# Kernel tuning notes

Measured on AMD Instinct MI355X. Metric: run time of the kernel, lower is better.

Reference implementation:

```python
import jax, jax.numpy as jnp
import numpy as np

N_NODES = 50000
N_EDGES = 400000
N_GRAPHS = 64
DN = 64    # node features
DE = 64    # edge features
DG = 16    # global features
DH = 128   # mlp hidden
DO = 64    # mlp output
NHID = 2   # hidden layers
E_IN = 2 * DN + DE + DG   # 208
N_IN = DN + DO + DG       # 144


def _mlp_params(key, d_in, d_h, d_out, n_hid):
    ks = jax.random.split(key, 3)
    w_in = jax.random.normal(ks[0], (d_in, d_h), jnp.float32) * (2.0 / d_in) ** 0.5
    w_h = jax.random.normal(ks[1], (n_hid, d_h, d_h), jnp.float32) * (2.0 / d_h) ** 0.5
    w_out = jax.random.normal(ks[2], (d_h, d_out), jnp.float32) * (2.0 / d_h) ** 0.5
    return (w_in, jnp.zeros((d_h,), jnp.float32), w_h, jnp.zeros((n_hid, d_h), jnp.float32),
            w_out, jnp.zeros((d_out,), jnp.float32), jnp.ones((d_out,), jnp.float32),
            jnp.zeros((d_out,), jnp.float32))


def _mlp(h, w_in, b_in, w_h, b_h, w_out, b_out, g, b):
    # Lin -> [relu, Lin]*NHID -> relu -> Lin -> LayerNorm  (dropout=0 at eval)
    h = h @ w_in + b_in
    for i in range(w_h.shape[0]):
        h = jax.nn.relu(h) @ w_h[i] + b_h[i]
    h = jax.nn.relu(h) @ w_out + b_out
    mu = jnp.mean(h, axis=-1, keepdims=True)
    var = jnp.mean((h - mu) ** 2, axis=-1, keepdims=True)
    return (h - mu) * jax.lax.rsqrt(var + 1e-5) * g + b


def setup_inputs() -> dict:
    key = jax.random.key(0)
    k = jax.random.split(key, 8)
    x = jax.random.normal(k[0], (N_NODES, DN), jnp.float32)
    edge_attr = jax.random.normal(k[1], (N_EDGES, DE), jnp.float32)
    u = jax.random.normal(k[2], (N_GRAPHS, DG), jnp.float32)
    edge_index = jax.random.randint(k[3], (2, N_EDGES), 0, N_NODES, dtype=jnp.int32)
    batch = jnp.sort(jax.random.randint(k[4], (N_NODES,), 0, N_GRAPHS, dtype=jnp.int32))
    names = ["w_in", "b_in", "w_h", "b_h", "w_out", "b_out", "ln_g", "ln_b"]
    d = {"x": x, "edge_attr": edge_attr, "u": u, "edge_index": edge_index, "batch": batch}
    for pref, kk, d_in in (("e_", k[5], E_IN), ("a_", k[6], E_IN), ("n_", k[7], N_IN)):
        for nm, v in zip(names, _mlp_params(kk, d_in, DH, DO, NHID)):
            d[pref + nm] = v
    return d


def reference(x, edge_attr, u, edge_index, batch,
              e_w_in, e_b_in, e_w_h, e_b_h, e_w_out, e_b_out, e_ln_g, e_ln_b,
              a_w_in, a_b_in, a_w_h, a_b_h, a_w_out, a_b_out, a_ln_g, a_ln_b,
              n_w_in, n_b_in, n_w_h, n_b_h, n_w_out, n_b_out, n_ln_g, n_ln_b):
    src, tgt = edge_index[0], edge_index[1]
    edge_batch = batch[src]
    # EdgeModel: gather src/tgt node feats + global feats, concat, MLP (+ sigmoid attention MLP)
    neigh = jnp.concatenate([x[src], x[tgt], edge_attr, u[edge_batch]], axis=1)  # [E, E_IN]
    e_out = _mlp(neigh, e_w_in, e_b_in, e_w_h, e_b_h, e_w_out, e_b_out, e_ln_g, e_ln_b)
    attn = jax.nn.sigmoid(_mlp(neigh, a_w_in, a_b_in, a_w_h, a_b_h, a_w_out, a_b_out, a_ln_g, a_ln_b))
    e_out = e_out * attn  # [E, DO]
    # NodeModel: scatter-sum incoming (target-indexed) edge outputs, concat, MLP
    agg = jax.ops.segment_sum(e_out, tgt, num_segments=x.shape[0])  # [N, DO], zeros for isolated nodes
    node_in = jnp.concatenate([x, agg, u[batch]], axis=1)  # [N, N_IN]
    x_out = _mlp(node_in, n_w_in, n_b_in, n_w_h, n_b_h, n_w_out, n_b_out, n_ln_g, n_ln_b)
    return x_out
```

## Files before the change

kernel.cpp:

```cpp
#include <hip/hip_runtime.h>
#include <math.h>

#define N_NODES 50000
#define N_EDGES 400000

typedef _Float16 half8 __attribute__((ext_vector_type(8)));
typedef float f32x4 __attribute__((ext_vector_type(4)));

#define LD1 232
#define LDH 136
#define LDN 168

#define AGG_OFF 0
#define XH_OFF  12800000
#define UH_OFF  19200000
#define WP_OFF  19202048
#define O_EW1 0
#define O_EH0 28672
#define O_EH1 45056
#define O_EWO 61440
#define O_AW1 69632
#define O_AH0 98304
#define O_AH1 114688
#define O_AWO 131072
#define O_NW1 139264
#define O_NH0 159744
#define O_NH1 176128
#define O_NWO 192512

__device__ __forceinline__ f32x4 mfma16(half8 a, half8 b, f32x4 c) {
  return __builtin_amdgcn_mfma_f32_16x16x32_f16(a, b, c, 0, 0, 0);
}

template<int NS, int LDSRC>
__device__ __forceinline__ void gemm32(const _Float16* __restrict__ src,
                                       _Float16* __restrict__ dst,
                                       const _Float16* __restrict__ wp16,
                                       const float* __restrict__ bias,
                                       int w, int lane) {
  const half8* wp = (const half8*)wp16;
  const int r = lane & 15, ch = lane >> 4;
  half8 B0[NS], B1[NS];
#pragma unroll
  for (int s = 0; s < NS; ++s) {
    B0[s] = wp[(s * 4 + ch) * 128 + w * 32 + r];
    B1[s] = wp[(s * 4 + ch) * 128 + w * 32 + 16 + r];
  }
  f32x4 a0[4], a1[4];
#pragma unroll
  for (int m = 0; m < 4; ++m) {
    a0[m] = (f32x4){0.f, 0.f, 0.f, 0.f};
    a1[m] = (f32x4){0.f, 0.f, 0.f, 0.f};
  }
#pragma unroll
  for (int s = 0; s < NS; ++s) {
#pragma unroll
    for (int m = 0; m < 4; ++m) {
      half8 a = *(const half8*)(src + (m * 16 + r) * LDSRC + s * 32 + ch * 8);
      a0[m] = mfma16(a, B0[s], a0[m]);
      a1[m] = mfma16(a, B1[s], a1[m]);
    }
  }
  float bb0 = bias[w * 32 + r], bb1 = bias[w * 32 + 16 + r];
#pragma unroll
  for (int m = 0; m < 4; ++m)
#pragma unroll
    for (int q = 0; q < 4; ++q) {
      int row = m * 16 + ch * 4 + q;
      dst[row * LDH + w * 32 + r]      = (_Float16)fmaxf(a0[m][q] + bb0, 0.f);
      dst[row * LDH + w * 32 + 16 + r] = (_Float16)fmaxf(a1[m][q] + bb1, 0.f);
    }
}

struct EdgeP {
  const float* edge_attr; const int* edge_index; const int* batch;
  const _Float16* x_h; const _Float16* u_h; const _Float16* wp;
  const float *eBin, *eBh, *eBout, *eG, *eBt;
  const float *aBin, *aBh, *aBout, *aG, *aBt;
  float* agg;
};

__global__ __launch_bounds__(512, 4) void edge_kernel(EdgeP p) {
  __shared__ __align__(16) _Float16 sIn[64 * LD1];
  __shared__ __align__(16) _Float16 sQe[64 * LDH];
  __shared__ __align__(16) _Float16 sQa[64 * LDH];
  __shared__ __align__(16) _Float16 sPa[64 * LDH];
  const int tid = threadIdx.x;
  const int e0 = blockIdx.x * 64;

  for (int idx = tid; idx < 64 * 32; idx += 512) {
    int c = idx & 31, e = idx >> 5;
    if (c >= 28) continue;
    int col = c * 8;
    half8 v;
    if (col < 64) {
      int s = p.edge_index[e0 + e];
      v = *(const half8*)(p.x_h + (size_t)s * 64 + col);
    } else if (col < 128) {
      int t = p.edge_index[N_EDGES + e0 + e];
      v = *(const half8*)(p.x_h + (size_t)t * 64 + col - 64);
    } else if (col < 192) {
      const float* ea = p.edge_attr + (size_t)(e0 + e) * 64 + (col - 128);
      float4 f0 = *(const float4*)ea, f1 = *(const float4*)(ea + 4);
      v[0] = (_Float16)f0.x; v[1] = (_Float16)f0.y;
      v[2] = (_Float16)f0.z; v[3] = (_Float16)f0.w;
      v[4] = (_Float16)f1.x; v[5] = (_Float16)f1.y;
      v[6] = (_Float16)f1.z; v[7] = (_Float16)f1.w;
    } else if (col < 208) {
      int s = p.edge_index[e0 + e];
      int eb = p.batch[s];
      v = *(const half8*)(p.u_h + eb * 16 + col - 192);
    } else {
#pragma unroll
      for (int j = 0; j < 8; ++j) v[j] = (_Float16)0.f;
    }
    *(half8*)(sIn + e * LD1 + col) = v;
  }
  __syncthreads();

  const int lane = tid & 63, wid = tid >> 6, we = wid & 3;
  const bool isE = wid < 4;
  _Float16* ping = isE ? sQe : sQa;
  _Float16* pong = isE ? sIn : sPa;
  const _Float16* w1 = p.wp + (isE ? O_EW1 : O_AW1);
  const _Float16* h0 = p.wp + (isE ? O_EH0 : O_AH0);
  const _Float16* h1 = p.wp + (isE ? O_EH1 : O_AH1);
  const _Float16* wo = p.wp + (isE ? O_EWO : O_AWO);
  const float* bin = isE ? p.eBin : p.aBin;
  const float* bh  = isE ? p.eBh  : p.aBh;
  const float* bo  = isE ? p.eBout: p.aBout;
  const float* g   = isE ? p.eG   : p.aG;
  const float* bt  = isE ? p.eBt  : p.aBt;

  gemm32<7, LD1>(sIn,  ping, w1, bin,      we, lane); __syncthreads();
  gemm32<4, LDH>(ping, pong, h0, bh,       we, lane); __syncthreads();
  gemm32<4, LDH>(pong, ping, h1, bh + 128, we, lane); __syncthreads();

  const int r = lane & 15, ch = lane >> 4;
  const half8* wpo = (const half8*)wo;
  half8 BO[4][4];
#pragma unroll
  for (int s = 0; s < 4; ++s)
#pragma unroll
    for (int t = 0; t < 4; ++t)
      BO[s][t] = wpo[(s * 4 + ch) * 64 + t * 16 + r];
  f32x4 acc[4];
#pragma unroll
  for (int t = 0; t < 4; ++t) acc[t] = (f32x4){0.f, 0.f, 0.f, 0.f};
#pragma unroll
  for (int s = 0; s < 4; ++s) {
    half8 a = *(const half8*)(ping + (we * 16 + r) * LDH + s * 32 + ch * 8);
#pragma unroll
    for (int t = 0; t < 4; ++t)
      acc[t] = mfma16(a, BO[s][t], acc[t]);
  }
  float gg[4], tt[4];
#pragma unroll
  for (int t = 0; t < 4; ++t) {
    int cidx = t * 16 + r;
    float bov = bo[cidx];
#pragma unroll
    for (int q = 0; q < 4; ++q) acc[t][q] += bov;
    gg[t] = g[cidx]; tt[t] = bt[cidx];
  }
  float mu_[4], rs_[4];
#pragma unroll
  for (int q = 0; q < 4; ++q) {
    float s1 = 0.f, s2 = 0.f;
#pragma unroll
    for (int t = 0; t < 4; ++t) { float v = acc[t][q]; s1 += v; s2 += v * v; }
#pragma unroll
    for (int mk = 1; mk < 16; mk <<= 1) {
      s1 += __shfl_xor(s1, mk); s2 += __shfl_xor(s2, mk);
    }
    mu_[q] = s1 * (1.f / 64);
    rs_[q] = rsqrtf(s2 * (1.f / 64) - mu_[q] * mu_[q] + 1e-5f);
  }
  float* cmb = (float*)sPa;
  if (!isE) {
#pragma unroll
    for (int q = 0; q < 4; ++q) {
      int row = we * 16 + ch * 4 + q;
#pragma unroll
      for (int t = 0; t < 4; ++t) {
        float oa = (acc[t][q] - mu_[q]) * rs_[q] * gg[t] + tt[t];
        cmb[row * 64 + t * 16 + r] = 1.f / (1.f + __expf(-oa));
      }
    }
  }
  __syncthreads();
  if (isE) {
#pragma unroll
    for (int q = 0; q < 4; ++q) {
      int row = we * 16 + ch * 4 + q;
      int tgt = p.edge_index[N_EDGES + e0 + row];
      float* ap = p.agg + (size_t)tgt * 64 + r;
#pragma unroll
      for (int t = 0; t < 4; ++t) {
        float oe = (acc[t][q] - mu_[q]) * rs_[q] * gg[t] + tt[t];
        atomicAdd(ap + t * 16, oe * cmb[row * 64 + t * 16 + r]);
      }
    }
  }
}

struct NodeP {
  const float* agg; const _Float16* x_h; const _Float16* u_h;
  const _Float16* wp; const int* batch;
  const float *Bin, *Bh, *Bout, *G, *Bt;
  float* out;
};

__global__ __launch_bounds__(256, 4) void node_kernel(NodeP p) {
  __shared__ __align__(16) _Float16 sIn[64 * LDN];
  __shared__ __align__(16) _Float16 sQ[64 * LDH];
  __shared__ int sB[64];
  const int tid = threadIdx.x;
  const int n0 = blockIdx.x * 64;

  if (tid < 64) {
    int n = n0 + tid;
    sB[tid] = (n < N_NODES) ? p.batch[n] : 0;
  }
  __syncthreads();

  for (int idx = tid; idx < 64 * 32; idx += 256) {
    int c = idx & 31, e = idx >> 5;
    if (c >= 21) continue;
    int n = n0 + e, col = c * 8;
    half8 v;
    if (n >= N_NODES || col >= 144) {
#pragma unroll
      for (int j = 0; j < 8; ++j) v[j] = (_Float16)0.f;
    } else if (col < 64) {
      v = *(const half8*)(p.x_h + (size_t)n * 64 + col);
    } else if (col < 128) {
      const float* ag = p.agg + (size_t)n * 64 + (col - 64);
      float4 f0 = *(const float4*)ag, f1 = *(const float4*)(ag + 4);
      v[0] = (_Float16)f0.x; v[1] = (_Float16)f0.y;
      v[2] = (_Float16)f0.z; v[3] = (_Float16)f0.w;
      v[4] = (_Float16)f1.x; v[5] = (_Float16)f1.y;
      v[6] = (_Float16)f1.z; v[7] = (_Float16)f1.w;
    } else {
      v = *(const half8*)(p.u_h + sB[e] * 16 + col - 128);
    }
    *(half8*)(sIn + e * LDN + col) = v;
  }
  __syncthreads();

  const int lane = tid & 63, w = tid >> 6;
  _Float16* sP = sIn;

  gemm32<5, LDN>(sIn, sQ, p.wp + O_NW1, p.Bin, w, lane);      __syncthreads();
  gemm32<4, LDH>(sQ, sP, p.wp + O_NH0, p.Bh, w, lane);        __syncthreads();
  gemm32<4, LDH>(sP, sQ, p.wp + O_NH1, p.Bh + 128, w, lane);  __syncthreads();

  const int r = lane & 15, ch = lane >> 4;
  const half8* wpNo = (const half8*)(p.wp + O_NWO);
  half8 BO[4][4];
#pragma unroll
  for (int s = 0; s < 4; ++s)
#pragma unroll
    for (int t = 0; t < 4; ++t)
      BO[s][t] = wpNo[(s * 4 + ch) * 64 + t * 16 + r];
  f32x4 acc[4];
#pragma unroll
  for (int t = 0; t < 4; ++t) acc[t] = (f32x4){0.f, 0.f, 0.f, 0.f};
#pragma unroll
  for (int s = 0; s < 4; ++s) {
    half8 h = *(const half8*)(sQ + (w * 16 + r) * LDH + s * 32 + ch * 8);
#pragma unroll
    for (int t = 0; t < 4; ++t)
      acc[t] = mfma16(h, BO[s][t], acc[t]);
  }
  float g[4], bt[4];
#pragma unroll
  for (int t = 0; t < 4; ++t) {
    int cidx = t * 16 + r;
    float bov = p.Bout[cidx];
#pragma unroll
    for (int q = 0; q < 4; ++q) acc[t][q] += bov;
    g[t] = p.G[cidx]; bt[t] = p.Bt[cidx];
  }
#pragma unroll
  for (int q = 0; q < 4; ++q) {
    float s1 = 0.f, s2 = 0.f;
#pragma unroll
    for (int t = 0; t < 4; ++t) { float v = acc[t][q]; s1 += v; s2 += v * v; }
#pragma unroll
    for (int mk = 1; mk < 16; mk <<= 1) {
      s1 += __shfl_xor(s1, mk); s2 += __shfl_xor(s2, mk);
    }
    float mu = s1 * (1.f / 64);
    float rs = rsqrtf(s2 * (1.f / 64) - mu * mu + 1e-5f);
    int row = w * 16 + ch * 4 + q;
    int n = n0 + row;
    if (n < N_NODES) {
#pragma unroll
      for (int t = 0; t < 4; ++t)
        p.out[(size_t)n * 64 + t * 16 + r] = (acc[t][q] - mu) * rs * g[t] + bt[t];
    }
  }
}

#define GX 112
struct PackP {
  const float* src[12];
  int Kreal[12], Nlog[12], size[12], dstoff[12];
  const float* x; const float* u;
  _Float16* x_h; _Float16* u_h; _Float16* wdst;
};

__global__ void pack_kernel(PackP p) {
  int y = blockIdx.y;
  int idx = blockIdx.x * 256 + threadIdx.x;
  if (y < 12) {
    int sz = p.size[y];
    if (idx >= sz) return;
    int N = 1 << p.Nlog[y];
    int j = idx & 7, t = idx >> 3;
    int n = t & (N - 1);
    int sc = t >> p.Nlog[y];
    int c = sc & 3, s = sc >> 2;
    int k = s * 32 + c * 8 + j;
    p.wdst[p.dstoff[y] + idx] =
        (k < p.Kreal[y]) ? (_Float16)p.src[y][k * N + n] : (_Float16)0.f;
  } else {
    for (int i = idx; i < N_NODES * 64; i += GX * 256) p.x_h[i] = (_Float16)p.x[i];
    for (int i = idx; i < 64 * 16; i += GX * 256) p.u_h[i] = (_Float16)p.u[i];
  }
}

extern "C" void kernel_launch(void* const* d_in, const int* in_sizes, int n_in,
                              void* d_out, int out_size, void* d_ws, size_t ws_size,
                              hipStream_t stream) {
  const float* x = (const float*)d_in[0];
  const float* edge_attr = (const float*)d_in[1];
  const float* u = (const float*)d_in[2];
  const int* edge_index = (const int*)d_in[3];
  const int* batch = (const int*)d_in[4];

  char* ws = (char*)d_ws;
  float* agg = (float*)(ws + AGG_OFF);
  _Float16* x_h = (_Float16*)(ws + XH_OFF);
  _Float16* u_h = (_Float16*)(ws + UH_OFF);
  _Float16* wp = (_Float16*)(ws + WP_OFF);

  hipMemsetAsync(agg, 0, (size_t)N_NODES * 64 * sizeof(float), stream);

  PackP pk;
  const float* eWh = (const float*)d_in[7];
  const float* aWh = (const float*)d_in[15];
  const float* nWh = (const float*)d_in[23];
  const float* srcs[12] = {
      (const float*)d_in[5], eWh, eWh + 16384, (const float*)d_in[9],
      (const float*)d_in[13], aWh, aWh + 16384, (const float*)d_in[17],
      (const float*)d_in[21], nWh, nWh + 16384, (const float*)d_in[25]};
  const int kr[12] = {208, 128, 128, 128, 208, 128, 128, 128, 144, 128, 128, 128};
  const int nl[12] = {7, 7, 7, 6, 7, 7, 7, 6, 7, 7, 7, 6};
  const int sz[12] = {28672, 16384, 16384, 8192, 28672, 16384, 16384, 8192,
                      20480, 16384, 16384, 8192};
  const int off[12] = {O_EW1, O_EH0, O_EH1, O_EWO, O_AW1, O_AH0, O_AH1, O_AWO,
                       O_NW1, O_NH0, O_NH1, O_NWO};
  for (int i = 0; i < 12; ++i) {
    pk.src[i] = srcs[i]; pk.Kreal[i] = kr[i]; pk.Nlog[i] = nl[i];
    pk.size[i] = sz[i]; pk.dstoff[i] = off[i];
  }
  pk.x = x; pk.u = u; pk.x_h = x_h; pk.u_h = u_h; pk.wdst = wp;
  pack_kernel<<<dim3(GX, 13), 256, 0, stream>>>(pk);

  EdgeP ep;
  ep.edge_attr = edge_attr; ep.edge_index = edge_index; ep.batch = batch;
  ep.x_h = x_h; ep.u_h = u_h; ep.wp = wp;
  ep.eBin = (const float*)d_in[6];  ep.eBh = (const float*)d_in[8];
  ep.eBout = (const float*)d_in[10]; ep.eG = (const float*)d_in[11];
  ep.eBt = (const float*)d_in[12];
  ep.aBin = (const float*)d_in[14]; ep.aBh = (const float*)d_in[16];
  ep.aBout = (const float*)d_in[18]; ep.aG = (const float*)d_in[19];
  ep.aBt = (const float*)d_in[20];
  ep.agg = agg;
  edge_kernel<<<N_EDGES / 64, 512, 0, stream>>>(ep);

  NodeP np;
  np.agg = agg; np.x_h = x_h; np.u_h = u_h; np.wp = wp; np.batch = batch;
  np.Bin = (const float*)d_in[22]; np.Bh = (const float*)d_in[24];
  np.Bout = (const float*)d_in[26]; np.G = (const float*)d_in[27];
  np.Bt = (const float*)d_in[28];
  np.out = (float*)d_out;
  node_kernel<<<(N_NODES + 63) / 64, 256, 0, stream>>>(np);
}
```

Baseline: 550.8 us.

## Load first-layer operands directly into registers and serialize edge/attention MLPs per block

Result: slower. 605.5 us (+9.9%).

```diff
diff --git a/kernel.cpp b/kernel.cpp
--- a/kernel.cpp
+++ b/kernel.cpp
@@ -3,13 +3,10 @@
 
 #define N_NODES 50000
 #define N_EDGES 400000
+#define LDH 136
 
 typedef _Float16 half8 __attribute__((ext_vector_type(8)));
 typedef float f32x4 __attribute__((ext_vector_type(4)));
-
-#define LD1 232
-#define LDH 136
-#define LDN 168
 
 #define AGG_OFF 0
 #define XH_OFF  12800000
@@ -32,13 +29,26 @@
   return __builtin_amdgcn_mfma_f32_16x16x32_f16(a, b, c, 0, 0, 0);
 }
 
-template<int NS, int LDSRC>
-__device__ __forceinline__ void gemm32(const _Float16* __restrict__ src,
+__device__ __forceinline__ half8 cvt8(float4 a, float4 b) {
+  half8 v;
+  v[0] = (_Float16)a.x; v[1] = (_Float16)a.y; v[2] = (_Float16)a.z; v[3] = (_Float16)a.w;
+  v[4] = (_Float16)b.x; v[5] = (_Float16)b.y; v[6] = (_Float16)b.z; v[7] = (_Float16)b.w;
+  return v;
+}
+
+__device__ __forceinline__ half8 zero8() {
+  half8 v;
+#pragma unroll
+  for (int j = 0; j < 8; ++j) v[j] = (_Float16)0.f;
+  return v;
+}
+
+template<int NS>
+__device__ __forceinline__ void gemm_h(const _Float16* __restrict__ src,
                                        _Float16* __restrict__ dst,
-                                       const _Float16* __restrict__ wp16,
+                                       const half8* __restrict__ wp,
                                        const float* __restrict__ bias,
                                        int w, int lane) {
-  const half8* wp = (const half8*)wp16;
   const int r = lane & 15, ch = lane >> 4;
   half8 B0[NS], B1[NS];
 #pragma unroll
@@ -46,6 +56,7 @@
     B0[s] = wp[(s * 4 + ch) * 128 + w * 32 + r];
     B1[s] = wp[(s * 4 + ch) * 128 + w * 32 + 16 + r];
   }
+  __builtin_amdgcn_sched_barrier(0);
   f32x4 a0[4], a1[4];
 #pragma unroll
   for (int m = 0; m < 4; ++m) {
@@ -56,7 +67,7 @@
   for (int s = 0; s < NS; ++s) {
 #pragma unroll
     for (int m = 0; m < 4; ++m) {
-      half8 a = *(const half8*)(src + (m * 16 + r) * LDSRC + s * 32 + ch * 8);
+      half8 a = *(const half8*)(src + (m * 16 + r) * LDH + s * 32 + ch * 8);
       a0[m] = mfma16(a, B0[s], a0[m]);
       a1[m] = mfma16(a, B1[s], a1[m]);
     }
@@ -70,6 +81,98 @@
       dst[row * LDH + w * 32 + r]      = (_Float16)fmaxf(a0[m][q] + bb0, 0.f);
       dst[row * LDH + w * 32 + 16 + r] = (_Float16)fmaxf(a1[m][q] + bb1, 0.f);
     }
+}
+
+__device__ __forceinline__ void l1_edge(const _Float16* __restrict__ x_h,
+                                        const float* __restrict__ edge_attr,
+                                        const _Float16* __restrict__ u_h,
+                                        const half8* __restrict__ wp,
+                                        const float* __restrict__ bias,
+                                        _Float16* __restrict__ dst,
+                                        const int* srcm, const int* tgtm, const int* ebm,
+                                        int e0, int w, int lane) {
+  const int r = lane & 15, ch = lane >> 4;
+  half8 B0[7], B1[7];
+#pragma unroll
+  for (int s = 0; s < 7; ++s) {
+    B0[s] = wp[(s * 4 + ch) * 128 + w * 32 + r];
+    B1[s] = wp[(s * 4 + ch) * 128 + w * 32 + 16 + r];
+  }
+  __builtin_amdgcn_sched_barrier(0);
+  float bb0 = bias[w * 32 + r], bb1 = bias[w * 32 + 16 + r];
+#pragma unroll
+  for (int g = 0; g < 2; ++g) {
+    half8 A[2][7];
+#pragma unroll
+    for (int mm = 0; mm < 2; ++mm) {
+      int m = g * 2 + mm;
+      const _Float16* xs = x_h + (size_t)srcm[m] * 64 + ch * 8;
+      const _Float16* xt = x_h + (size_t)tgtm[m] * 64 + ch * 8;
+      A[mm][0] = *(const half8*)(xs);
+      A[mm][1] = *(const half8*)(xs + 32);
+      A[mm][2] = *(const half8*)(xt);
+      A[mm][3] = *(const half8*)(xt + 32);
+      const float* ea = edge_attr + (size_t)(e0 + m * 16 + r) * 64 + ch * 8;
+      float4 f0 = *(const float4*)(ea);
+      float4 f1 = *(const float4*)(ea + 4);
+      float4 f2 = *(const float4*)(ea + 32);
+      float4 f3 = *(const float4*)(ea + 36);
+      A[mm][4] = cvt8(f0, f1);
+      A[mm][5] = cvt8(f2, f3);
+      half8 vu = zero8();
+      if (ch < 2) vu = *(const half8*)(u_h + ebm[m] * 16 + ch * 8);
+      A[mm][6] = vu;
+    }
+    __builtin_amdgcn_sched_barrier(0);
+    f32x4 a0[2], a1[2];
+#pragma unroll
+    for (int mm = 0; mm < 2; ++mm) {
+      a0[mm] = (f32x4){0.f, 0.f, 0.f, 0.f};
+      a1[mm] = (f32x4){0.f, 0.f, 0.f, 0.f};
+    }
+#pragma unroll
+    for (int s = 0; s < 7; ++s)
+#pragma unroll
+      for (int mm = 0; mm < 2; ++mm) {
+        a0[mm] = mfma16(A[mm][s], B0[s], a0[mm]);
+        a1[mm] = mfma16(A[mm][s], B1[s], a1[mm]);
+      }
+#pragma unroll
+    for (int mm = 0; mm < 2; ++mm)
+#pragma unroll
+      for (int q = 0; q < 4; ++q) {
+        int row = (g * 2 + mm) * 16 + ch * 4 + q;
+        dst[row * LDH + w * 32 + r]      = (_Float16)fmaxf(a0[mm][q] + bb0, 0.f);
+        dst[row * LDH + w * 32 + 16 + r] = (_Float16)fmaxf(a1[mm][q] + bb1, 0.f);
+      }
+  }
+}
+
+__device__ __forceinline__ void out_gemm(const _Float16* __restrict__ src,
+                                         const half8* __restrict__ wpo,
+                                         const float* __restrict__ bo,
+                                         f32x4 acc[4], int w, int lane) {
+  const int r = lane & 15, ch = lane >> 4;
+  half8 BO[4][4];
+#pragma unroll
+  for (int s = 0; s < 4; ++s)
+#pragma unroll
+    for (int t = 0; t < 4; ++t) BO[s][t] = wpo[(s * 4 + ch) * 64 + t * 16 + r];
+  __builtin_amdgcn_sched_barrier(0);
+#pragma unroll
+  for (int t = 0; t < 4; ++t) acc[t] = (f32x4){0.f, 0.f, 0.f, 0.f};
+#pragma unroll
+  for (int s = 0; s < 4; ++s) {
+    half8 a = *(const half8*)(src + (w * 16 + r) * LDH + s * 32 + ch * 8);
+#pragma unroll
+    for (int t = 0; t < 4; ++t) acc[t] = mfma16(a, BO[s][t], acc[t]);
+  }
+#pragma unroll
+  for (int t = 0; t < 4; ++t) {
+    float bv = bo[t * 16 + r];
+#pragma unroll
+    for (int q = 0; q < 4; ++q) acc[t][q] += bv;
+  }
 }
 
 struct EdgeP {
@@ -80,125 +183,84 @@
   float* agg;
 };
 
-__global__ __launch_bounds__(512, 4) void edge_kernel(EdgeP p) {
-  __shared__ __align__(16) _Float16 sIn[64 * LD1];
-  __shared__ __align__(16) _Float16 sQe[64 * LDH];
-  __shared__ __align__(16) _Float16 sQa[64 * LDH];
-  __shared__ __align__(16) _Float16 sPa[64 * LDH];
-  const int tid = threadIdx.x;
+__global__ __launch_bounds__(256, 3) void edge_kernel(EdgeP p) {
+  __shared__ __align__(16) _Float16 sA[64 * LDH];
+  __shared__ __align__(16) _Float16 sB[64 * LDH];
+  __shared__ __align__(16) _Float16 sC[64 * LDH];
+  const int tid = threadIdx.x, lane = tid & 63, w = tid >> 6;
+  const int r = lane & 15, ch = lane >> 4;
   const int e0 = blockIdx.x * 64;
 
-  for (int idx = tid; idx < 64 * 32; idx += 512) {
-    int c = idx & 31, e = idx >> 5;
-    if (c >= 28) continue;
-    int col = c * 8;
-    half8 v;
-    if (col < 64) {
-      int s = p.edge_index[e0 + e];
-      v = *(const half8*)(p.x_h + (size_t)s * 64 + col);
-    } else if (col < 128) {
-      int t = p.edge_index[N_EDGES + e0 + e];
-      v = *(const half8*)(p.x_h + (size_t)t * 64 + col - 64);
-    } else if (col < 192) {
-      const float* ea = p.edge_attr + (size_t)(e0 + e) * 64 + (col - 128);
-      float4 f0 = *(const float4*)ea, f1 = *(const float4*)(ea + 4);
-      v[0] = (_Float16)f0.x; v[1] = (_Float16)f0.y;
-      v[2] = (_Float16)f0.z; v[3] = (_Float16)f0.w;
-      v[4] = (_Float16)f1.x; v[5] = (_Float16)f1.y;
-      v[6] = (_Float16)f1.z; v[7] = (_Float16)f1.w;
-    } else if (col < 208) {
-      int s = p.edge_index[e0 + e];
-      int eb = p.batch[s];
-      v = *(const half8*)(p.u_h + eb * 16 + col - 192);
-    } else {
-#pragma unroll
-      for (int j = 0; j < 8; ++j) v[j] = (_Float16)0.f;
-    }
-    *(half8*)(sIn + e * LD1 + col) = v;
-  }
+  int srcm[4], tgtm[4], ebm[4];
+#pragma unroll
+  for (int m = 0; m < 4; ++m) srcm[m] = p.edge_index[e0 + m * 16 + r];
+#pragma unroll
+  for (int m = 0; m < 4; ++m) tgtm[m] = p.edge_index[N_EDGES + e0 + m * 16 + r];
+#pragma unroll
+  for (int m = 0; m < 4; ++m) ebm[m] = p.batch[srcm[m]];
+
+  l1_edge(p.x_h, p.edge_attr, p.u_h, (const half8*)(p.wp + O_EW1), p.eBin, sA,
+          srcm, tgtm, ebm, e0, w, lane);
   __syncthreads();
-
-  const int lane = tid & 63, wid = tid >> 6, we = wid & 3;
-  const bool isE = wid < 4;
-  _Float16* ping = isE ? sQe : sQa;
-  _Float16* pong = isE ? sIn : sPa;
-  const _Float16* w1 = p.wp + (isE ? O_EW1 : O_AW1);
-  const _Float16* h0 = p.wp + (isE ? O_EH0 : O_AH0);
-  const _Float16* h1 = p.wp + (isE ? O_EH1 : O_AH1);
-  const _Float16* wo = p.wp + (isE ? O_EWO : O_AWO);
-  const float* bin = isE ? p.eBin : p.aBin;
-  const float* bh  = isE ? p.eBh  : p.aBh;
-  const float* bo  = isE ? p.eBout: p.aBout;
-  const float* g   = isE ? p.eG   : p.aG;
-  const float* bt  = isE ? p.eBt  : p.aBt;
-
-  gemm32<7, LD1>(sIn,  ping, w1, bin,      we, lane); __syncthreads();
-  gemm32<4, LDH>(ping, pong, h0, bh,       we, lane); __syncthreads();
-  gemm32<4, LDH>(pong, ping, h1, bh + 128, we, lane); __syncthreads();
-
-  const int r = lane & 15, ch = lane >> 4;
-  const half8* wpo = (const half8*)wo;
-  half8 BO[4][4];
-#pragma unroll
-  for (int s = 0; s < 4; ++s)
-#pragma unroll
-    for (int t = 0; t < 4; ++t)
-      BO[s][t] = wpo[(s * 4 + ch) * 64 + t * 16 + r];
-  f32x4 acc[4];
-#pragma unroll
-  for (int t = 0; t < 4; ++t) acc[t] = (f32x4){0.f, 0.f, 0.f, 0.f};
-#pragma unroll
-  for (int s = 0; s < 4; ++s) {
-    half8 a = *(const half8*)(ping + (we * 16 + r) * LDH + s * 32 + ch * 8);
-#pragma unroll
-    for (int t = 0; t < 4; ++t)
-      acc[t] = mfma16(a, BO[s][t], acc[t]);
-  }
-  float gg[4], tt[4];
-#pragma unroll
-  for (int t = 0; t < 4; ++t) {
-    int cidx = t * 16 + r;
-    float bov = bo[cidx];
-#pragma unroll
-    for (int q = 0; q < 4; ++q) acc[t][q] += bov;
-    gg[t] = g[cidx]; tt[t] = bt[cidx];
-  }
-  float mu_[4], rs_[4];
-#pragma unroll
-  for (int q = 0; q < 4; ++q) {
-    float s1 = 0.f, s2 = 0.f;
-#pragma unroll
-    for (int t = 0; t < 4; ++t) { float v = acc[t][q]; s1 += v; s2 += v * v; }
-#pragma unroll
-    for (int mk = 1; mk < 16; mk <<= 1) {
-      s1 += __shfl_xor(s1, mk); s2 += __shfl_xor(s2, mk);
-    }
-    mu_[q] = s1 * (1.f / 64);
-    rs_[q] = rsqrtf(s2 * (1.f / 64) - mu_[q] * mu_[q] + 1e-5f);
-  }
-  float* cmb = (float*)sPa;
-  if (!isE) {
+  gemm_h<4>(sA, sB, (const half8*)(p.wp + O_EH0), p.eBh, w, lane);       __syncthreads();
+  gemm_h<4>(sB, sA, (const half8*)(p.wp + O_EH1), p.eBh + 128, w, lane); __syncthreads();
+
+  float* bufE = (float*)sB;
+  {
+    f32x4 acc[4];
+    out_gemm(sA, (const half8*)(p.wp + O_EWO), p.eBout, acc, w, lane);
+    float g4[4], b4[4];
+#pragma unroll
+    for (int t = 0; t < 4; ++t) { g4[t] = p.eG[t * 16 + r]; b4[t] = p.eBt[t * 16 + r]; }
 #pragma unroll
     for (int q = 0; q < 4; ++q) {
-      int row = we * 16 + ch * 4 + q;
+      float s1 = 0.f, s2 = 0.f;
+#pragma unroll
+      for (int t = 0; t < 4; ++t) { float v = acc[t][q]; s1 += v; s2 += v * v; }
+#pragma unroll
+      for (int mk = 1; mk < 16; mk <<= 1) { s1 += __shfl_xor(s1, mk); s2 += __shfl_xor(s2, mk); }
+      float mu = s1 * (1.f / 64);
+      float rs = rsqrtf(s2 * (1.f / 64) - mu * mu + 1e-5f);
+      int row = w * 16 + ch * 4 + q;
+#pragma unroll
+      for (int t = 0; t < 4; ++t)
+        bufE[row * 68 + t * 16 + r] = (acc[t][q] - mu) * rs * g4[t] + b4[t];
+    }
+  }
+  __syncthreads();
+
+  l1_edge(p.x_h, p.edge_attr, p.u_h, (const half8*)(p.wp + O_AW1), p.aBin, sC,
+          srcm, tgtm, ebm, e0, w, lane);
+  __syncthreads();
+  gemm_h<4>(sC, sA, (const half8*)(p.wp + O_AH0), p.aBh, w, lane);       __syncthreads();
+  gemm_h<4>(sA, sC, (const half8*)(p.wp + O_AH1), p.aBh + 128, w, lane); __syncthreads();
+
+  {
+    f32x4 acc[4];
+    out_gemm(sC, (const half8*)(p.wp + O_AWO), p.aBout, acc, w, lane);
+    float g4[4], b4[4];
+#pragma unroll
+    for (int t = 0; t < 4; ++t) { g4[t] = p.aG[t * 16 + r]; b4[t] = p.aBt[t * 16 + r]; }
+    int tq[4];
+#pragma unroll
+    for (int q = 0; q < 4; ++q)
+      tq[q] = p.edge_index[N_EDGES + e0 + w * 16 + ch * 4 + q];
+#pragma unroll
+    for (int q = 0; q < 4; ++q) {
+      float s1 = 0.f, s2 = 0.f;
+#pragma unroll
+      for (int t = 0; t < 4; ++t) { float v = acc[t][q]; s1 += v; s2 += v * v; }
+#pragma unroll
+      for (int mk = 1; mk < 16; mk <<= 1) { s1 += __shfl_xor(s1, mk); s2 += __shfl_xor(s2, mk); }
+      float mu = s1 * (1.f / 64);
+      float rs = rsqrtf(s2 * (1.f / 64) - mu * mu + 1e-5f);
+      int row = w * 16 + ch * 4 + q;
+      float* ap = p.agg + (size_t)tq[q] * 64 + r;
 #pragma unroll
       for (int t = 0; t < 4; ++t) {
-        float oa = (acc[t][q] - mu_[q]) * rs_[q] * gg[t] + tt[t];
-        cmb[row * 64 + t * 16 + r] = 1.f / (1.f + __expf(-oa));
-      }
-    }
-  }
-  __syncthreads();
-  if (isE) {
-#pragma unroll
-    for (int q = 0; q < 4; ++q) {
-      int row = we * 16 + ch * 4 + q;
-      int tgt = p.edge_index[N_EDGES + e0 + row];
-      float* ap = p.agg + (size_t)tgt * 64 + r;
-#pragma unroll
-      for (int t = 0; t < 4; ++t) {
-        float oe = (acc[t][q] - mu_[q]) * rs_[q] * gg[t] + tt[t];
-        atomicAdd(ap + t * 16, oe * cmb[row * 64 + t * 16 + r]);
+        float oa = (acc[t][q] - mu) * rs * g4[t] + b4[t];
+        float sg = 1.f / (1.f + __expf(-oa));
+        atomicAdd(ap + t * 16, bufE[row * 68 + t * 16 + r] * sg);
       }
     }
   }
@@ -211,86 +273,90 @@
   float* out;
 };
 
+__device__ __forceinline__ void l1_node(const NodeP& p,
+                                        _Float16* __restrict__ dst,
+                                        int n0, int w, int lane) {
+  const int r = lane & 15, ch = lane >> 4;
+  const half8* wp = (const half8*)(p.wp + O_NW1);
+  half8 B0[5], B1[5];
+#pragma unroll
+  for (int s = 0; s < 5; ++s) {
+    B0[s] = wp[(s * 4 + ch) * 128 + w * 32 + r];
+    B1[s] = wp[(s * 4 + ch) * 128 + w * 32 + 16 + r];
+  }
+  __builtin_amdgcn_sched_barrier(0);
+  float bb0 = p.Bin[w * 32 + r], bb1 = p.Bin[w * 32 + 16 + r];
+#pragma unroll
+  for (int g = 0; g < 2; ++g) {
+    half8 A[2][5];
+#pragma unroll
+    for (int mm = 0; mm < 2; ++mm) {
+      int m = g * 2 + mm;
+      int n = n0 + m * 16 + r;
+      int nn = (n < N_NODES) ? n : 0;
+      const _Float16* xs = p.x_h + (size_t)nn * 64 + ch * 8;
+      A[mm][0] = *(const half8*)(xs);
+      A[mm][1] = *(const half8*)(xs + 32);
+      const float* ag = p.agg + (size_t)nn * 64 + ch * 8;
+      float4 f0 = *(const float4*)(ag);
+      float4 f1 = *(const float4*)(ag + 4);
+      float4 f2 = *(const float4*)(ag + 32);
+      float4 f3 = *(const float4*)(ag + 36);
+      A[mm][2] = cvt8(f0, f1);
+      A[mm][3] = cvt8(f2, f3);
+      half8 vu = zero8();
+      if (ch < 2) vu = *(const half8*)(p.u_h + p.batch[nn] * 16 + ch * 8);
+      A[mm][4] = vu;
+    }
+    __builtin_amdgcn_sched_barrier(0);
+    f32x4 a0[2], a1[2];
+#pragma unroll
+    for (int mm = 0; mm < 2; ++mm) {
+      a0[mm] = (f32x4){0.f, 0.f, 0.f, 0.f};
+      a1[mm] = (f32x4){0.f, 0.f, 0.f, 0.f};
+    }
+#pragma unroll
+    for (int s = 0; s < 5; ++s)
+#pragma unroll
+      for (int mm = 0; mm < 2; ++mm) {
+        a0[mm] = mfma16(A[mm][s], B0[s], a0[mm]);
+        a1[mm] = mfma16(A[mm][s], B1[s], a1[mm]);
+      }
+#pragma unroll
+    for (int mm = 0; mm < 2; ++mm)
+#pragma unroll
+      for (int q = 0; q < 4; ++q) {
+        int row = (g * 2 + mm) * 16 + ch * 4 + q;
+        dst[row * LDH + w * 32 + r]      = (_Float16)fmaxf(a0[mm][q] + bb0, 0.f);
+        dst[row * LDH + w * 32 + 16 + r] = (_Float16)fmaxf(a1[mm][q] + bb1, 0.f);
+      }
+  }
+}
+
 __global__ __launch_bounds__(256, 4) void node_kernel(NodeP p) {
-  __shared__ __align__(16) _Float16 sIn[64 * LDN];
   __shared__ __align__(16) _Float16 sQ[64 * LDH];
-  __shared__ int sB[64];
-  const int tid = threadIdx.x;
+  __shared__ __align__(16) _Float16 sP[64 * LDH];
+  const int tid = threadIdx.x, lane = tid & 63, w = tid >> 6;
+  const int r = lane & 15, ch = lane >> 4;
   const int n0 = blockIdx.x * 64;
 
-  if (tid < 64) {
-    int n = n0 + tid;
-    sB[tid] = (n < N_NODES) ? p.batch[n] : 0;
-  }
+  l1_node(p, sQ, n0, w, lane);
   __syncthreads();
-
-  for (int idx = tid; idx < 64 * 32; idx += 256) {
-    int c = idx & 31, e = idx >> 5;
-    if (c >= 21) continue;
-    int n = n0 + e, col = c * 8;
-    half8 v;
-    if (n >= N_NODES || col >= 144) {
-#pragma unroll
-      for (int j = 0; j < 8; ++j) v[j] = (_Float16)0.f;
-    } else if (col < 64) {
-      v = *(const half8*)(p.x_h + (size_t)n * 64 + col);
-    } else if (col < 128) {
-      const float* ag = p.agg + (size_t)n * 64 + (col - 64);
-      float4 f0 = *(const float4*)ag, f1 = *(const float4*)(ag + 4);
-      v[0] = (_Float16)f0.x; v[1] = (_Float16)f0.y;
-      v[2] = (_Float16)f0.z; v[3] = (_Float16)f0.w;
-      v[4] = (_Float16)f1.x; v[5] = (_Float16)f1.y;
-      v[6] = (_Float16)f1.z; v[7] = (_Float16)f1.w;
-    } else {
-      v = *(const half8*)(p.u_h + sB[e] * 16 + col - 128);
-    }
-    *(half8*)(sIn + e * LDN + col) = v;
-  }
-  __syncthreads();
-
-  const int lane = tid & 63, w = tid >> 6;
-  _Float16* sP = sIn;
-
-  gemm32<5, LDN>(sIn, sQ, p.wp + O_NW1, p.Bin, w, lane);      __syncthreads();
-  gemm32<4, LDH>(sQ, sP, p.wp + O_NH0, p.Bh, w, lane);        __syncthreads();
-  gemm32<4, LDH>(sP, sQ, p.wp + O_NH1, p.Bh + 128, w, lane);  __syncthreads();
-
-  const int r = lane & 15, ch = lane >> 4;
-  const half8* wpNo = (const half8*)(p.wp + O_NWO);
-  half8 BO[4][4];
-#pragma unroll
-  for (int s = 0; s < 4; ++s)
-#pragma unroll
-    for (int t = 0; t < 4; ++t)
-      BO[s][t] = wpNo[(s * 4 + ch) * 64 + t * 16 + r];
+  gemm_h<4>(sQ, sP, (const half8*)(p.wp + O_NH0), p.Bh, w, lane);       __syncthreads();
+  gemm_h<4>(sP, sQ, (const half8*)(p.wp + O_NH1), p.Bh + 128, w, lane); __syncthreads();
+
   f32x4 acc[4];
-#pragma unroll
-  for (int t = 0; t < 4; ++t) acc[t] = (f32x4){0.f, 0.f, 0.f, 0.f};
-#pragma unroll
-  for (int s = 0; s < 4; ++s) {
-    half8 h = *(const half8*)(sQ + (w * 16 + r) * LDH + s * 32 + ch * 8);
-#pragma unroll
-    for (int t = 0; t < 4; ++t)
-      acc[t] = mfma16(h, BO[s][t], acc[t]);
-  }
-  float g[4], bt[4];
-#pragma unroll
-  for (int t = 0; t < 4; ++t) {
-    int cidx = t * 16 + r;
-    float bov = p.Bout[cidx];
-#pragma unroll
-    for (int q = 0; q < 4; ++q) acc[t][q] += bov;
-    g[t] = p.G[cidx]; bt[t] = p.Bt[cidx];
-  }
+  out_gemm(sQ, (const half8*)(p.wp + O_NWO), p.Bout, acc, w, lane);
+  float g4[4], b4[4];
+#pragma unroll
+  for (int t = 0; t < 4; ++t) { g4[t] = p.G[t * 16 + r]; b4[t] = p.Bt[t * 16 + r]; }
 #pragma unroll
   for (int q = 0; q < 4; ++q) {
     float s1 = 0.f, s2 = 0.f;
 #pragma unroll
     for (int t = 0; t < 4; ++t) { float v = acc[t][q]; s1 += v; s2 += v * v; }
 #pragma unroll
-    for (int mk = 1; mk < 16; mk <<= 1) {
-      s1 += __shfl_xor(s1, mk); s2 += __shfl_xor(s2, mk);
-    }
+    for (int mk = 1; mk < 16; mk <<= 1) { s1 += __shfl_xor(s1, mk); s2 += __shfl_xor(s2, mk); }
     float mu = s1 * (1.f / 64);
     float rs = rsqrtf(s2 * (1.f / 64) - mu * mu + 1e-5f);
     int row = w * 16 + ch * 4 + q;
@@ -298,7 +364,7 @@
     if (n < N_NODES) {
 #pragma unroll
       for (int t = 0; t < 4; ++t)
-        p.out[(size_t)n * 64 + t * 16 + r] = (acc[t][q] - mu) * rs * g[t] + bt[t];
+        p.out[(size_t)n * 64 + t * 16 + r] = (acc[t][q] - mu) * rs * g4[t] + b4[t];
     }
   }
 }
@@ -379,7 +445,7 @@
   ep.aBout = (const float*)d_in[18]; ep.aG = (const float*)d_in[19];
   ep.aBt = (const float*)d_in[20];
   ep.agg = agg;
-  edge_kernel<<<N_EDGES / 64, 512, 0, stream>>>(ep);
+  edge_kernel<<<N_EDGES / 64, 256, 0, stream>>>(ep);
 
   NodeP np;
   np.agg = agg; np.x_h = x_h; np.u_h = u_h; np.wp = wp; np.batch = batch;
```

## Shrink edge/node tiles to 32 rows and run edge and attention MLPs sequentially

Applied to the files above, without the earlier changes.

After: 564.6 us. 2.5% more time.

```diff
diff --git a/kernel.cpp b/kernel.cpp
--- a/kernel.cpp
+++ b/kernel.cpp
@@ -3,13 +3,12 @@
 
 #define N_NODES 50000
 #define N_EDGES 400000
-
-typedef _Float16 half8 __attribute__((ext_vector_type(8)));
-typedef float f32x4 __attribute__((ext_vector_type(4)));
-
 #define LD1 232
 #define LDH 136
 #define LDN 168
+
+typedef _Float16 half8 __attribute__((ext_vector_type(8)));
+typedef float f32x4 __attribute__((ext_vector_type(4)));
 
 #define AGG_OFF 0
 #define XH_OFF  12800000
@@ -32,13 +31,26 @@
   return __builtin_amdgcn_mfma_f32_16x16x32_f16(a, b, c, 0, 0, 0);
 }
 
+__device__ __forceinline__ half8 cvt8(float4 a, float4 b) {
+  half8 v;
+  v[0] = (_Float16)a.x; v[1] = (_Float16)a.y; v[2] = (_Float16)a.z; v[3] = (_Float16)a.w;
+  v[4] = (_Float16)b.x; v[5] = (_Float16)b.y; v[6] = (_Float16)b.z; v[7] = (_Float16)b.w;
+  return v;
+}
+
+__device__ __forceinline__ half8 zero8() {
+  half8 v;
+#pragma unroll
+  for (int j = 0; j < 8; ++j) v[j] = (_Float16)0.f;
+  return v;
+}
+
 template<int NS, int LDSRC>
-__device__ __forceinline__ void gemm32(const _Float16* __restrict__ src,
-                                       _Float16* __restrict__ dst,
-                                       const _Float16* __restrict__ wp16,
-                                       const float* __restrict__ bias,
-                                       int w, int lane) {
-  const half8* wp = (const half8*)wp16;
+__device__ __forceinline__ void gemm_m2(const _Float16* __restrict__ src,
+                                        _Float16* __restrict__ dst,
+                                        const half8* __restrict__ wp,
+                                        const float* __restrict__ bias,
+                                        int w, int lane) {
   const int r = lane & 15, ch = lane >> 4;
   half8 B0[NS], B1[NS];
 #pragma unroll
@@ -46,16 +58,16 @@
     B0[s] = wp[(s * 4 + ch) * 128 + w * 32 + r];
     B1[s] = wp[(s * 4 + ch) * 128 + w * 32 + 16 + r];
   }
-  f32x4 a0[4], a1[4];
-#pragma unroll
-  for (int m = 0; m < 4; ++m) {
+  f32x4 a0[2], a1[2];
+#pragma unroll
+  for (int m = 0; m < 2; ++m) {
     a0[m] = (f32x4){0.f, 0.f, 0.f, 0.f};
     a1[m] = (f32x4){0.f, 0.f, 0.f, 0.f};
   }
 #pragma unroll
   for (int s = 0; s < NS; ++s) {
 #pragma unroll
-    for (int m = 0; m < 4; ++m) {
+    for (int m = 0; m < 2; ++m) {
       half8 a = *(const half8*)(src + (m * 16 + r) * LDSRC + s * 32 + ch * 8);
       a0[m] = mfma16(a, B0[s], a0[m]);
       a1[m] = mfma16(a, B1[s], a1[m]);
@@ -63,13 +75,58 @@
   }
   float bb0 = bias[w * 32 + r], bb1 = bias[w * 32 + 16 + r];
 #pragma unroll
-  for (int m = 0; m < 4; ++m)
+  for (int m = 0; m < 2; ++m)
 #pragma unroll
     for (int q = 0; q < 4; ++q) {
       int row = m * 16 + ch * 4 + q;
       dst[row * LDH + w * 32 + r]      = (_Float16)fmaxf(a0[m][q] + bb0, 0.f);
       dst[row * LDH + w * 32 + 16 + r] = (_Float16)fmaxf(a1[m][q] + bb1, 0.f);
     }
+}
+
+__device__ __forceinline__ void out16(const _Float16* __restrict__ src,
+                                      const half8* __restrict__ wpo,
+                                      const float* __restrict__ bo,
+                                      const float* __restrict__ g,
+                                      const float* __restrict__ bt,
+                                      f32x4 acc[4], int w, int lane) {
+  const int r = lane & 15, ch = lane >> 4;
+  half8 BO[4][4];
+#pragma unroll
+  for (int s = 0; s < 4; ++s)
+#pragma unroll
+    for (int t = 0; t < 4; ++t) BO[s][t] = wpo[(s * 4 + ch) * 64 + t * 16 + r];
+#pragma unroll
+  for (int t = 0; t < 4; ++t) acc[t] = (f32x4){0.f, 0.f, 0.f, 0.f};
+#pragma unroll
+  for (int s = 0; s < 4; ++s) {
+    half8 a = *(const half8*)(src + (w * 16 + r) * LDH + s * 32 + ch * 8);
+#pragma unroll
+    for (int t = 0; t < 4; ++t) acc[t] = mfma16(a, BO[s][t], acc[t]);
+  }
+  float g4[4], b4[4];
+#pragma unroll
+  for (int t = 0; t < 4; ++t) {
+    float bv = bo[t * 16 + r];
+#pragma unroll
+    for (int q = 0; q < 4; ++q) acc[t][q] += bv;
+    g4[t] = g[t * 16 + r]; b4[t] = bt[t * 16 + r];
+  }
+#pragma unroll
+  for (int q = 0; q < 4; ++q) {
+    float s1 = 0.f, s2 = 0.f;
+#pragma unroll
+    for (int t = 0; t < 4; ++t) { float v = acc[t][q]; s1 += v; s2 += v * v; }
+#pragma unroll
+    for (int mk = 1; mk < 16; mk <<= 1) {
+      s1 += __shfl_xor(s1, mk); s2 += __shfl_xor(s2, mk);
+    }
+    float mu = s1 * (1.f / 64);
+    float rs = rsqrtf(s2 * (1.f / 64) - mu * mu + 1e-5f);
+#pragma unroll
+    for (int t = 0; t < 4; ++t)
+      acc[t][q] = (acc[t][q] - mu) * rs * g4[t] + b4[t];
+  }
 }
 
 struct EdgeP {
@@ -80,15 +137,15 @@
   float* agg;
 };
 
-__global__ __launch_bounds__(512, 4) void edge_kernel(EdgeP p) {
-  __shared__ __align__(16) _Float16 sIn[64 * LD1];
-  __shared__ __align__(16) _Float16 sQe[64 * LDH];
-  __shared__ __align__(16) _Float16 sQa[64 * LDH];
-  __shared__ __align__(16) _Float16 sPa[64 * LDH];
-  const int tid = threadIdx.x;
-  const int e0 = blockIdx.x * 64;
-
-  for (int idx = tid; idx < 64 * 32; idx += 512) {
+__global__ __launch_bounds__(256, 4) void edge_kernel(EdgeP p) {
+  __shared__ __align__(16) _Float16 sIn[32 * LD1];
+  __shared__ __align__(16) _Float16 sA[32 * LDH];
+  __shared__ __align__(16) _Float16 sB[32 * LDH];
+  const int tid = threadIdx.x, lane = tid & 63, w = tid >> 6;
+  const int r = lane & 15, ch = lane >> 4;
+  const int e0 = blockIdx.x * 32;
+
+  for (int idx = tid; idx < 32 * 32; idx += 256) {
     int c = idx & 31, e = idx >> 5;
     if (c >= 28) continue;
     int col = c * 8;
@@ -101,104 +158,57 @@
       v = *(const half8*)(p.x_h + (size_t)t * 64 + col - 64);
     } else if (col < 192) {
       const float* ea = p.edge_attr + (size_t)(e0 + e) * 64 + (col - 128);
-      float4 f0 = *(const float4*)ea, f1 = *(const float4*)(ea + 4);
-      v[0] = (_Float16)f0.x; v[1] = (_Float16)f0.y;
-      v[2] = (_Float16)f0.z; v[3] = (_Float16)f0.w;
-      v[4] = (_Float16)f1.x; v[5] = (_Float16)f1.y;
-      v[6] = (_Float16)f1.z; v[7] = (_Float16)f1.w;
+      v = cvt8(*(const float4*)ea, *(const float4*)(ea + 4));
     } else if (col < 208) {
       int s = p.edge_index[e0 + e];
       int eb = p.batch[s];
       v = *(const half8*)(p.u_h + eb * 16 + col - 192);
     } else {
-#pragma unroll
-      for (int j = 0; j < 8; ++j) v[j] = (_Float16)0.f;
+      v = zero8();
     }
     *(half8*)(sIn + e * LD1 + col) = v;
   }
   __syncthreads();
 
-  const int lane = tid & 63, wid = tid >> 6, we = wid & 3;
-  const bool isE = wid < 4;
-  _Float16* ping = isE ? sQe : sQa;
-  _Float16* pong = isE ? sIn : sPa;
-  const _Float16* w1 = p.wp + (isE ? O_EW1 : O_AW1);
-  const _Float16* h0 = p.wp + (isE ? O_EH0 : O_AH0);
-  const _Float16* h1 = p.wp + (isE ? O_EH1 : O_AH1);
-  const _Float16* wo = p.wp + (isE ? O_EWO : O_AWO);
-  const float* bin = isE ? p.eBin : p.aBin;
-  const float* bh  = isE ? p.eBh  : p.aBh;
-  const float* bo  = isE ? p.eBout: p.aBout;
-  const float* g   = isE ? p.eG   : p.aG;
-  const float* bt  = isE ? p.eBt  : p.aBt;
-
-  gemm32<7, LD1>(sIn,  ping, w1, bin,      we, lane); __syncthreads();
-  gemm32<4, LDH>(ping, pong, h0, bh,       we, lane); __syncthreads();
-  gemm32<4, LDH>(pong, ping, h1, bh + 128, we, lane); __syncthreads();
-
-  const int r = lane & 15, ch = lane >> 4;
-  const half8* wpo = (const half8*)wo;
-  half8 BO[4][4];
-#pragma unroll
-  for (int s = 0; s < 4; ++s)
-#pragma unroll
-    for (int t = 0; t < 4; ++t)
-      BO[s][t] = wpo[(s * 4 + ch) * 64 + t * 16 + r];
-  f32x4 acc[4];
-#pragma unroll
-  for (int t = 0; t < 4; ++t) acc[t] = (f32x4){0.f, 0.f, 0.f, 0.f};
-#pragma unroll
-  for (int s = 0; s < 4; ++s) {
-    half8 a = *(const half8*)(ping + (we * 16 + r) * LDH + s * 32 + ch * 8);
-#pragma unroll
-    for (int t = 0; t < 4; ++t)
-      acc[t] = mfma16(a, BO[s][t], acc[t]);
-  }
-  float gg[4], tt[4];
-#pragma unroll
-  for (int t = 0; t < 4; ++t) {
-    int cidx = t * 16 + r;
-    float bov = bo[cidx];
-#pragma unroll
-    for (int q = 0; q < 4; ++q) acc[t][q] += bov;
-    gg[t] = g[cidx]; tt[t] = bt[cidx];
-  }
-  float mu_[4], rs_[4];
-#pragma unroll
-  for (int q = 0; q < 4; ++q) {
-    float s1 = 0.f, s2 = 0.f;
-#pragma unroll
-    for (int t = 0; t < 4; ++t) { float v = acc[t][q]; s1 += v; s2 += v * v; }
-#pragma unroll
-    for (int mk = 1; mk < 16; mk <<= 1) {
-      s1 += __shfl_xor(s1, mk); s2 += __shfl_xor(s2, mk);
-    }
-    mu_[q] = s1 * (1.f / 64);
-    rs_[q] = rsqrtf(s2 * (1.f / 64) - mu_[q] * mu_[q] + 1e-5f);
-  }
-  float* cmb = (float*)sPa;
-  if (!isE) {
+  gemm_m2<7, LD1>(sIn, sA, (const half8*)(p.wp + O_EW1), p.eBin, w, lane);
+  __syncthreads();
+  gemm_m2<4, LDH>(sA, sB, (const half8*)(p.wp + O_EH0), p.eBh, w, lane);
+  __syncthreads();
+  gemm_m2<4, LDH>(sB, sA, (const half8*)(p.wp + O_EH1), p.eBh + 128, w, lane);
+  __syncthreads();
+  half8 eP0 = zero8(), eP1 = zero8();
+  if (w < 2) {
+    f32x4 aE[4];
+    out16(sA, (const half8*)(p.wp + O_EWO), p.eBout, p.eG, p.eBt, aE, w, lane);
 #pragma unroll
     for (int q = 0; q < 4; ++q) {
-      int row = we * 16 + ch * 4 + q;
+      eP0[q] = (_Float16)aE[0][q]; eP0[4 + q] = (_Float16)aE[1][q];
+      eP1[q] = (_Float16)aE[2][q]; eP1[4 + q] = (_Float16)aE[3][q];
+    }
+  }
+  __syncthreads();
+
+  gemm_m2<7, LD1>(sIn, sA, (const half8*)(p.wp + O_AW1), p.aBin, w, lane);
+  __syncthreads();
+  gemm_m2<4, LDH>(sA, sB, (const half8*)(p.wp + O_AH0), p.aBh, w, lane);
+  __syncthreads();
+  gemm_m2<4, LDH>(sB, sA, (const half8*)(p.wp + O_AH1), p.aBh + 128, w, lane);
+  __syncthreads();
+  if (w < 2) {
+    f32x4 aA[4];
+    out16(sA, (const half8*)(p.wp + O_AWO), p.aBout, p.aG, p.aBt, aA, w, lane);
+    int tq[4];
+#pragma unroll
+    for (int q = 0; q < 4; ++q)
+      tq[q] = p.edge_index[N_EDGES + e0 + w * 16 + ch * 4 + q];
+#pragma unroll
+    for (int q = 0; q < 4; ++q) {
+      float* ap = p.agg + (size_t)tq[q] * 64 + r;
 #pragma unroll
       for (int t = 0; t < 4; ++t) {
-        float oa = (acc[t][q] - mu_[q]) * rs_[q] * gg[t] + tt[t];
-        cmb[row * 64 + t * 16 + r] = 1.f / (1.f + __expf(-oa));
-      }
-    }
-  }
-  __syncthreads();
-  if (isE) {
-#pragma unroll
-    for (int q = 0; q < 4; ++q) {
-      int row = we * 16 + ch * 4 + q;
-      int tgt = p.edge_index[N_EDGES + e0 + row];
-      float* ap = p.agg + (size_t)tgt * 64 + r;
-#pragma unroll
-      for (int t = 0; t < 4; ++t) {
-        float oe = (acc[t][q] - mu_[q]) * rs_[q] * gg[t] + tt[t];
-        atomicAdd(ap + t * 16, oe * cmb[row * 64 + t * 16 + r]);
+        float sg = 1.f / (1.f + __expf(-aA[t][q]));
+        float oe = (t < 2) ? (float)eP0[t * 4 + q] : (float)eP1[(t - 2) * 4 + q];
+        atomicAdd(ap + t * 16, oe * sg);
       }
     }
   }
@@ -212,93 +222,49 @@
 };
 
 __global__ __launch_bounds__(256, 4) void node_kernel(NodeP p) {
-  __shared__ __align__(16) _Float16 sIn[64 * LDN];
-  __shared__ __align__(16) _Float16 sQ[64 * LDH];
-  __shared__ int sB[64];
-  const int tid = threadIdx.x;
-  const int n0 = blockIdx.x * 64;
-
-  if (tid < 64) {
-    int n = n0 + tid;
-    sB[tid] = (n < N_NODES) ? p.batch[n] : 0;
-  }
-  __syncthreads();
-
-  for (int idx = tid; idx < 64 * 32; idx += 256) {
+  __shared__ __align__(16) _Float16 sIn[32 * LDN];
+  __shared__ __align__(16) _Float16 sA[32 * LDH];
+  __shared__ __align__(16) _Float16 sB[32 * LDH];
+  const int tid = threadIdx.x, lane = tid & 63, w = tid >> 6;
+  const int r = lane & 15, ch = lane >> 4;
+  const int n0 = blockIdx.x * 32;
+
+  for (int idx = tid; idx < 32 * 32; idx += 256) {
     int c = idx & 31, e = idx >> 5;
-    if (c >= 21) continue;
+    if (c >= 20) continue;
     int n = n0 + e, col = c * 8;
     half8 v;
     if (n >= N_NODES || col >= 144) {
-#pragma unroll
-      for (int j = 0; j < 8; ++j) v[j] = (_Float16)0.f;
+      v = zero8();
     } else if (col < 64) {
       v = *(const half8*)(p.x_h + (size_t)n * 64 + col);
     } else if (col < 128) {
       const float* ag = p.agg + (size_t)n * 64 + (col - 64);
-      float4 f0 = *(const float4*)ag, f1 = *(const float4*)(ag + 4);
-      v[0] = (_Float16)f0.x; v[1] = (_Float16)f0.y;
-      v[2] = (_Float16)f0.z; v[3] = (_Float16)f0.w;
-      v[4] = (_Float16)f1.x; v[5] = (_Float16)f1.y;
-      v[6] = (_Float16)f1.z; v[7] = (_Float16)f1.w;
+      v = cvt8(*(const float4*)ag, *(const float4*)(ag + 4));
     } else {
-      v = *(const half8*)(p.u_h + sB[e] * 16 + col - 128);
+      v = *(const half8*)(p.u_h + p.batch[n] * 16 + col - 128);
     }
     *(half8*)(sIn + e * LDN + col) = v;
   }
   __syncthreads();
 
-  const int lane = tid & 63, w = tid >> 6;
-  _Float16* sP = sIn;
-
-  gemm32<5, LDN>(sIn, sQ, p.wp + O_NW1, p.Bin, w, lane);      __syncthreads();
-  gemm32<4, LDH>(sQ, sP, p.wp + O_NH0, p.Bh, w, lane);        __syncthreads();
-  gemm32<4, LDH>(sP, sQ, p.wp + O_NH1, p.Bh + 128, w, lane);  __syncthreads();
-
-  const int r = lane & 15, ch = lane >> 4;
-  const half8* wpNo = (const half8*)(p.wp + O_NWO);
-  half8 BO[4][4];
-#pragma unroll
-  for (int s = 0; s < 4; ++s)
-#pragma unroll
-    for (int t = 0; t < 4; ++t)
-      BO[s][t] = wpNo[(s * 4 + ch) * 64 + t * 16 + r];
-  f32x4 acc[4];
-#pragma unroll
-  for (int t = 0; t < 4; ++t) acc[t] = (f32x4){0.f, 0.f, 0.f, 0.f};
-#pragma unroll
-  for (int s = 0; s < 4; ++s) {
-    half8 h = *(const half8*)(sQ + (w * 16 + r) * LDH + s * 32 + ch * 8);
-#pragma unroll
-    for (int t = 0; t < 4; ++t)
-      acc[t] = mfma16(h, BO[s][t], acc[t]);
-  }
-  float g[4], bt[4];
-#pragma unroll
-  for (int t = 0; t < 4; ++t) {
-    int cidx = t * 16 + r;
-    float bov = p.Bout[cidx];
-#pragma unroll
-    for (int q = 0; q < 4; ++q) acc[t][q] += bov;
-    g[t] = p.G[cidx]; bt[t] = p.Bt[cidx];
-  }
-#pragma unroll
-  for (int q = 0; q < 4; ++q) {
-    float s1 = 0.f, s2 = 0.f;
-#pragma unroll
-    for (int t = 0; t < 4; ++t) { float v = acc[t][q]; s1 += v; s2 += v * v; }
-#pragma unroll
-    for (int mk = 1; mk < 16; mk <<= 1) {
-      s1 += __shfl_xor(s1, mk); s2 += __shfl_xor(s2, mk);
-    }
-    float mu = s1 * (1.f / 64);
-    float rs = rsqrtf(s2 * (1.f / 64) - mu * mu + 1e-5f);
-    int row = w * 16 + ch * 4 + q;
-    int n = n0 + row;
-    if (n < N_NODES) {
-#pragma unroll
-      for (int t = 0; t < 4; ++t)
-        p.out[(size_t)n * 64 + t * 16 + r] = (acc[t][q] - mu) * rs * g[t] + bt[t];
+  gemm_m2<5, LDN>(sIn, sA, (const half8*)(p.wp + O_NW1), p.Bin, w, lane);
+  __syncthreads();
+  gemm_m2<4, LDH>(sA, sB, (const half8*)(p.wp + O_NH0), p.Bh, w, lane);
+  __syncthreads();
+  gemm_m2<4, LDH>(sB, sA, (const half8*)(p.wp + O_NH1), p.Bh + 128, w, lane);
+  __syncthreads();
+  if (w < 2) {
+    f32x4 acc[4];
+    out16(sA, (const half8*)(p.wp + O_NWO), p.Bout, p.G, p.Bt, acc, w, lane);
+#pragma unroll
+    for (int q = 0; q < 4; ++q) {
+      int n = n0 + w * 16 + ch * 4 + q;
+      if (n < N_NODES) {
+#pragma unroll
+        for (int t = 0; t < 4; ++t)
+          p.out[(size_t)n * 64 + t * 16 + r] = acc[t][q];
+      }
     }
   }
 }
@@ -379,7 +345,7 @@
   ep.aBout = (const float*)d_in[18]; ep.aG = (const float*)d_in[19];
   ep.aBt = (const float*)d_in[20];
   ep.agg = agg;
-  edge_kernel<<<N_EDGES / 64, 512, 0, stream>>>(ep);
+  edge_kernel<<<N_EDGES / 32, 256, 0, stream>>>(ep);
 
   NodeP np;
   np.agg = agg; np.x_h = x_h; np.u_h = u_h; np.wp = wp; np.batch = batch;
@@ -387,5 +353,5 @@
   np.Bout = (const float*)d_in[26]; np.G = (const float*)d_in[27];
   np.Bt = (const float*)d_in[28];
   np.out = (float*)d_out;
-  node_kernel<<<(N_NODES + 63) / 64, 256, 0, stream>>>(np);
-}
+  node_kernel<<<(N_NODES + 31) / 32, 256, 0, stream>>>(np);
+}
```
